# Kernel optimization log

Measured on AMD Instinct MI355X. Metric: run time of the kernel, lower is better.

## Reference

```python
import jax, jax.numpy as jnp
import numpy as np

B, T, C = 1, 1024, 2048
N = 64          # head_size
H = C // N      # 32 heads
D_W = 96        # max(32, round(1.8*sqrt(C)/32)*32)
D_A = 96
D_V = 64        # max(32, round(1.3*sqrt(C)/32)*32)
EPS = 1e-12     # F.normalize eps


def setup_inputs() -> dict:
    key = jax.random.key(0)
    ks = jax.random.split(key, 24)
    g = lambda i, shape, s=0.02: jax.random.normal(ks[i], shape, jnp.float32) * s
    return {
        "x": jax.random.normal(ks[0], (B, T, C), jnp.float32),
        "v_first": jax.random.normal(ks[1], (B, T, C), jnp.float32),
        "attention_mask": jnp.ones((B, T), jnp.float32),
        "w0": g(2, (1, 1, C), 0.1) - 0.5,
        "w1": g(3, (C, D_W)),
        "w2": g(4, (D_W, C)),
        "a0": g(5, (1, 1, C), 0.1),
        "a1": g(6, (C, D_A)),
        "a2": g(7, (D_A, C)),
        "v0": g(8, (1, 1, C), 0.1) + 1.0,
        "v1": g(9, (C, D_V)),
        "v2": g(10, (D_V, C)),
        "k_k": jnp.full((1, 1, C), 0.85, jnp.float32),
        "k_a": jnp.ones((1, 1, C), jnp.float32),
        "r_k": g(11, (H, N), 0.1),
        "Wr": g(12, (C, C)),   # pre-transposed Linear weights: y = x @ W
        "Wk": g(13, (C, C)),
        "Wv": g(14, (C, C)),
        "Wo": g(15, (C, C)),
    }


def rwkv7_scan(r, w, k, v, a, b, mask):
    """RWKV-7 recurrence (RUN_CUDA_RWKV7g). All of r,w,k,v,a,b are (B,T,C); mask (B,T).
    Per head: S_t = S_{t-1}*diag(exp(-exp(w_t))) + (S_{t-1} a_t) b_t^T + v_t k_t^T,
    out_t = S_t r_t.  Masked timesteps leave the state untouched."""
    rh, kh, vh, ah, bh = (t.reshape(B, T, H, N) for t in (r, k, v, a, b))
    dec = jnp.exp(-jnp.exp(w.reshape(B, T, H, N)))
    m = mask[:, :, None, None]
    dec = dec * m + (1.0 - m)            # no decay on padded steps
    kh, vh, ah, bh = kh * m, vh * m, ah * m, bh * m
    seq = tuple(jnp.moveaxis(t, 1, 0) for t in (dec, rh, kh, vh, ah, bh))
    s0 = jnp.zeros((B, H, N, N), r.dtype)  # state[...,i,j]: i=value dim, j=key dim

    def step(state, inp):
        d, rr, kk, vv, aa, bb = inp      # each (B,H,N)
        sa = jnp.einsum('bhij,bhj->bhi', state, aa)
        state = (state * d[:, :, None, :]
                 + sa[..., None] * bb[:, :, None, :]
                 + vv[..., None] * kk[:, :, None, :])
        return state, jnp.einsum('bhij,bhj->bhi', state, rr)

    _, out = jax.lax.scan(step, s0, seq)
    return jnp.moveaxis(out, 0, 1).reshape(B, T, C)


def reference(x, v_first, attention_mask, w0, w1, w2, a0, a1, a2,
              v0, v1, v2, k_k, k_a, r_k, Wr, Wk, Wv, Wo):
    r = x @ Wr
    k = x @ Wk
    v = x @ Wv
    w = -jax.nn.softplus(-(w0 + jnp.tanh(x @ w1) @ w2)) - 0.6
    # layer_id != 0: mix with v_first
    v = v + (v_first - v) * jax.nn.sigmoid(v0 + (x @ v1) @ v2)
    a = jax.nn.sigmoid(a0 + (x @ a1) @ a2)
    kk = k * k_k
    kkh = kk.reshape(B, T, H, N)
    kkh = kkh / jnp.maximum(jnp.linalg.norm(kkh, axis=-1, keepdims=True), EPS)
    kk = kkh.reshape(B, T, C)
    k = k * (1.0 + (a - 1.0) * k_a)
    o = rwkv7_scan(r, w, k, v, -kk, kk * a, attention_mask)
    rh, kh, vh = (t.reshape(B, T, H, N) for t in (r, k, v))
    o = o + ((rh * kh * r_k).sum(-1, keepdims=True) * vh).reshape(B, T, C)
    return (o @ Wo, v_first)
```

## Files before the change

### kernel.cpp

```cpp
#include <hip/hip_runtime.h>
#include <math.h>

#define T_LEN 1024
#define C_DIM 2048
#define H_N   32
#define HEAD  64
#define BTC   (T_LEN * C_DIM)
#define REC2  768
#define RKV_N 6144
#define NPAIR (T_LEN / 2)

typedef __attribute__((ext_vector_type(8))) __bf16 bf16x8;
typedef __attribute__((ext_vector_type(4))) float  f32x4;

__device__ __forceinline__ void gll16(const void* g, void* l) {
    __builtin_amdgcn_global_load_lds((const __attribute__((address_space(1))) void*)g,
                                     (__attribute__((address_space(3))) void*)l, 16, 0, 0);
}

__device__ __forceinline__ float hex_add(float x) {
    int a = __builtin_amdgcn_mov_dpp(__float_as_int(x), 0xB1, 0xF, 0xF, true);
    float y = x + __int_as_float(a);
    int b = __builtin_amdgcn_mov_dpp(__float_as_int(y), 0x4E, 0xF, 0xF, true);
    float z = y + __int_as_float(b);
    int c = __builtin_amdgcn_mov_dpp(__float_as_int(z), 0x141, 0xF, 0xF, true);
    float w = z + __int_as_float(c);
    int d = __builtin_amdgcn_mov_dpp(__float_as_int(w), 0x140, 0xF, 0xF, true);
    return w + __int_as_float(d);
}

__global__ void cast_bf16_k(const float* __restrict__ s, __bf16* __restrict__ d, int n) {
    int i = blockIdx.x * 256 + threadIdx.x;
    if (i < n) d[i] = (__bf16)s[i];
}

__global__ void act_lora1_k(const float* __restrict__ s, __bf16* __restrict__ d) {
    int i = blockIdx.x * 256 + threadIdx.x;
    float v = s[i];
    if ((i & 255) < 96) v = tanhf(v);
    d[i] = (__bf16)v;
}

struct TransBatch {
    const float* s[10];
    __bf16*      d[10];
    int R[10];
    int C[10];
};
__global__ void transpose_batch_k(TransBatch tb) {
    int z = blockIdx.z;
    const float* src = tb.s[z];
    __bf16* dst = tb.d[z];
    int R = tb.R[z], C = tb.C[z];
    int c0 = blockIdx.x * 32, r0 = blockIdx.y * 32;
    if (c0 >= C || r0 >= R) return;
    __shared__ float tile[32][33];
    int tx = threadIdx.x, ty = threadIdx.y;
#pragma unroll
    for (int i = 0; i < 32; i += 8)
        tile[ty + i][tx] = src[(size_t)(r0 + ty + i) * C + c0 + tx];
    __syncthreads();
#pragma unroll
    for (int i = 0; i < 32; i += 8)
        dst[(size_t)(c0 + ty + i) * R + r0 + tx] = (__bf16)tile[tx][ty + i];
}

__global__ __launch_bounds__(256) void gemm_lds_64x128(
    const __bf16* __restrict__ A, const __bf16* __restrict__ BT,
    float* __restrict__ O, int M, int N, int K) {
    __shared__ __bf16 As[64 * 32];
    __shared__ __bf16 Bs[128 * 32];
    int tid  = threadIdx.x;
    int lane = tid & 63;
    int wv   = tid >> 6;
    int m    = lane & 15;
    int q    = lane >> 4;
    int wr   = wv >> 1, wc = wv & 1;
    int row0 = blockIdx.x * 64;
    int col0 = blockIdx.y * 128;

    int srow  = tid >> 2;
    int skoff = (tid & 3) * 8;
    const __bf16* agp = A  + (size_t)(row0 + srow) * K + skoff;
    const __bf16* bgp = BT + (size_t)(col0 + srow) * K + skoff;
    __bf16* alp = As + (size_t)(tid & ~63) * 8;
    __bf16* blp = Bs + (size_t)(tid & ~63) * 8;

    f32x4 acc[2][4];
#pragma unroll
    for (int i = 0; i < 2; i++)
#pragma unroll
        for (int j = 0; j < 4; j++) acc[i][j] = {0.f, 0.f, 0.f, 0.f};

    for (int k0 = 0; k0 < K; k0 += 32) {
        gll16(agp + k0, alp);
        gll16(bgp + k0, blp);
        gll16(bgp + (size_t)64 * K + k0, blp + 64 * 32);
        __syncthreads();

        bf16x8 af[2], bfv[4];
#pragma unroll
        for (int i = 0; i < 2; i++)
            af[i] = *(const bf16x8*)&As[(wr * 32 + i * 16 + m) * 32 + q * 8];
#pragma unroll
        for (int j = 0; j < 4; j++)
            bfv[j] = *(const bf16x8*)&Bs[(wc * 64 + j * 16 + m) * 32 + q * 8];
#pragma unroll
        for (int i = 0; i < 2; i++)
#pragma unroll
            for (int j = 0; j < 4; j++)
                acc[i][j] = __builtin_amdgcn_mfma_f32_16x16x32_bf16(af[i], bfv[j], acc[i][j], 0, 0, 0);
        __syncthreads();
    }

#pragma unroll
    for (int i = 0; i < 2; i++) {
        int orow = row0 + wr * 32 + i * 16 + q * 4;
#pragma unroll
        for (int j = 0; j < 4; j++) {
            int ocol = col0 + wc * 64 + j * 16 + m;
#pragma unroll
            for (int t = 0; t < 4; t++)
                O[(size_t)(orow + t) * N + ocol] = acc[i][j][t];
        }
    }
}

__global__ __launch_bounds__(256) void gemm_lds_128x128(
    const __bf16* __restrict__ A, const __bf16* __restrict__ BT,
    float* __restrict__ O, int M, int N, int K) {
    __shared__ __bf16 As[128 * 32];
    __shared__ __bf16 Bs[128 * 32];
    int tid  = threadIdx.x;
    int lane = tid & 63;
    int wv   = tid >> 6;
    int m    = lane & 15;
    int q    = lane >> 4;
    int row0 = blockIdx.x * 128;
    int col0 = blockIdx.y * 128;

    int srow  = tid >> 2;
    int skoff = (tid & 3) * 8;
    const __bf16* agp = A  + (size_t)(row0 + srow) * K + skoff;
    const __bf16* bgp = BT + (size_t)(col0 + srow) * K + skoff;
    __bf16* alp = As + (size_t)(tid & ~63) * 8;
    __bf16* blp = Bs + (size_t)(tid & ~63) * 8;

    f32x4 acc[2][8];
#pragma unroll
    for (int i = 0; i < 2; i++)
#pragma unroll
        for (int j = 0; j < 8; j++) acc[i][j] = {0.f, 0.f, 0.f, 0.f};

    for (int k0 = 0; k0 < K; k0 += 32) {
        gll16(agp + k0, alp);
        gll16(agp + (size_t)64 * K + k0, alp + 64 * 32);
        gll16(bgp + k0, blp);
        gll16(bgp + (size_t)64 * K + k0, blp + 64 * 32);
        __syncthreads();

        bf16x8 af[2], bfv[8];
#pragma unroll
        for (int i = 0; i < 2; i++)
            af[i] = *(const bf16x8*)&As[(wv * 32 + i * 16 + m) * 32 + q * 8];
#pragma unroll
        for (int j = 0; j < 8; j++)
            bfv[j] = *(const bf16x8*)&Bs[(j * 16 + m) * 32 + q * 8];
#pragma unroll
        for (int i = 0; i < 2; i++)
#pragma unroll
            for (int j = 0; j < 8; j++)
                acc[i][j] = __builtin_amdgcn_mfma_f32_16x16x32_bf16(af[i], bfv[j], acc[i][j], 0, 0, 0);
        __syncthreads();
    }

#pragma unroll
    for (int i = 0; i < 2; i++) {
        int orow = row0 + wv * 32 + i * 16 + q * 4;
#pragma unroll
        for (int j = 0; j < 8; j++) {
            int ocol = col0 + j * 16 + m;
#pragma unroll
            for (int t = 0; t < 4; t++)
                O[(size_t)(orow + t) * N + ocol] = acc[i][j][t];
        }
    }
}

struct Lora2Cfg {
    const __bf16* A[3];
    const __bf16* BT[3];
    float*        O[3];
    int K[3];
};
__global__ __launch_bounds__(256) void gemm_lora2_k(Lora2Cfg cfg) {
    const int LDA = 256, N = C_DIM;
    int z = blockIdx.z;
    const __bf16* A  = cfg.A[z];
    const __bf16* BT = cfg.BT[z];
    float* O = cfg.O[z];
    int K = cfg.K[z];

    __shared__ __bf16 As[64 * 32];
    __shared__ __bf16 Bs[128 * 32];
    int tid  = threadIdx.x;
    int lane = tid & 63;
    int wv   = tid >> 6;
    int m    = lane & 15;
    int q    = lane >> 4;
    int wr   = wv >> 1, wc = wv & 1;
    int row0 = blockIdx.x * 64;
    int col0 = blockIdx.y * 128;

    int srow  = tid >> 2;
    int skoff = (tid & 3) * 8;
    const __bf16* agp = A  + (size_t)(row0 + srow) * LDA + skoff;
    const __bf16* bgp = BT + (size_t)(col0 + srow) * K + skoff;
    __bf16* alp = As + (size_t)(tid & ~63) * 8;
    __bf16* blp = Bs + (size_t)(tid & ~63) * 8;

    f32x4 acc[2][4];
#pragma unroll
    for (int i = 0; i < 2; i++)
#pragma unroll
        for (int j = 0; j < 4; j++) acc[i][j] = {0.f, 0.f, 0.f, 0.f};

    for (int k0 = 0; k0 < K; k0 += 32) {
        gll16(agp + k0, alp);
        gll16(bgp + k0, blp);
        gll16(bgp + (size_t)64 * K + k0, blp + 64 * 32);
        __syncthreads();

        bf16x8 af[2], bfv[4];
#pragma unroll
        for (int i = 0; i < 2; i++)
            af[i] = *(const bf16x8*)&As[(wr * 32 + i * 16 + m) * 32 + q * 8];
#pragma unroll
        for (int j = 0; j < 4; j++)
            bfv[j] = *(const bf16x8*)&Bs[(wc * 64 + j * 16 + m) * 32 + q * 8];
#pragma unroll
        for (int i = 0; i < 2; i++)
#pragma unroll
            for (int j = 0; j < 4; j++)
                acc[i][j] = __builtin_amdgcn_mfma_f32_16x16x32_bf16(af[i], bfv[j], acc[i][j], 0, 0, 0);
        __syncthreads();
    }

#pragma unroll
    for (int i = 0; i < 2; i++) {
        int orow = row0 + wr * 32 + i * 16 + q * 4;
#pragma unroll
        for (int j = 0; j < 4; j++) {
            int ocol = col0 + wc * 64 + j * 16 + m;
#pragma unroll
            for (int t = 0; t < 4; t++)
                O[(size_t)(orow + t) * N + ocol] = acc[i][j][t];
        }
    }
}

__global__ __launch_bounds__(64) void gemm_bt_w16(
    const __bf16* __restrict__ A, const __bf16* __restrict__ BT,
    float* __restrict__ O, int M, int N, int K) {
    int lane = threadIdx.x & 63;
    int m = lane & 15, q = lane >> 4;
    int row0 = blockIdx.x * 16;
    int col0 = blockIdx.y * 16;
    const __bf16* ap = A  + (size_t)(row0 + m) * K + q * 8;
    const __bf16* bp = BT + (size_t)(col0 + m) * K + q * 8;
    f32x4 acc = {0.f,0.f,0.f,0.f};
    for (int k0 = 0; k0 < K; k0 += 32) {
        bf16x8 av = *(const bf16x8*)(ap + k0);
        bf16x8 bv = *(const bf16x8*)(bp + k0);
        acc = __builtin_amdgcn_mfma_f32_16x16x32_bf16(av, bv, acc, 0, 0, 0);
    }
    int orow = row0 + q * 4;
    int ocol = col0 + m;
#pragma unroll
    for (int i = 0; i < 4; i++)
        O[(size_t)(orow + i) * N + ocol] = acc[i];
}

__global__ __launch_bounds__(64) void prep2_k(
    float* __restrict__ rkv,
    const float* __restrict__ vfirst,
    const float* __restrict__ ywb, const float* __restrict__ yab,
    const float* __restrict__ yvb,
    float* __restrict__ pk,
    const float* __restrict__ w0, const float* __restrict__ a0,
    const float* __restrict__ v0, const float* __restrict__ k_k,
    const float* __restrict__ k_a, const float* __restrict__ amask) {
    int tp = blockIdx.x >> 5;
    int h  = blockIdx.x & 31;
    int n  = threadIdx.x;
    int cc = h * HEAD + n;

    float d[2], a[2], bv[2], k[2], v[2], r[2];
#pragma unroll
    for (int s = 0; s < 2; ++s) {
        int t = 2 * tp + s;
        int idx = t * C_DIM + cc;
        size_t idx6 = (size_t)t * RKV_N + cc;
        float m  = amask[t];
        float rr = rkv[idx6];
        float kv = rkv[idx6 + 2048];
        float vv = rkv[idx6 + 4096];
        float wv = w0[cc] + ywb[idx];
        float wfin = -log1pf(expf(-wv)) - 0.6f;
        float dec  = expf(-expf(wfin));
        float sv   = 1.f / (1.f + expf(-(v0[cc] + yvb[idx])));
        float vnew = fmaf(vfirst[idx] - vv, sv, vv);
        float av   = 1.f / (1.f + expf(-(a0[cc] + yab[idx])));
        float kkp  = kv * k_k[cc];
        float ss = kkp * kkp;
#pragma unroll
        for (int off = 32; off > 0; off >>= 1) ss += __shfl_xor(ss, off);
        float kkn  = kkp / fmaxf(sqrtf(ss), 1e-12f);
        float knew = kv * (1.f + (av - 1.f) * k_a[cc]);
        d[s]  = dec * m + (1.f - m);
        a[s]  = -kkn * m;
        bv[s] = kkn * av * m;
        k[s]  = knew * m;
        v[s]  = vnew * m;
        r[s]  = rr;
        rkv[idx6 + 2048] = knew;
        rkv[idx6 + 4096] = vnew;
    }

    float dba = bv[0] * a[1];
    float dka = k[0]  * a[1];
    float dbr = bv[0] * r[0];
    float dkr = k[0]  * r[0];
#pragma unroll
    for (int off = 32; off > 0; off >>= 1) {
        dba += __shfl_xor(dba, off);
        dka += __shfl_xor(dka, off);
        dbr += __shfl_xor(dbr, off);
        dkr += __shfl_xor(dkr, off);
    }

    size_t rec = ((size_t)tp * H_N + h) * REC2;
    pk[rec + n]        = a[0];
    pk[rec + 64 + n]   = d[0] * a[1];
    pk[rec + 128 + n]  = fmaf(dbr, a[0], d[0] * r[0]);
    pk[rec + 192 + n]  = d[0] * d[1];
    pk[rec + 256 + n]  = fmaf(dba, bv[1], d[1] * bv[0]);
    pk[rec + 320 + n]  = bv[1];
    pk[rec + 384 + n]  = fmaf(dka, bv[1], d[1] * k[0]);
    pk[rec + 448 + n]  = k[1];
    pk[rec + 512 + n]  = r[1];
    pk[rec + 576 + n * 3]     = v[0];
    pk[rec + 576 + n * 3 + 1] = v[1];
    pk[rec + 576 + n * 3 + 2] = dkr * v[0];
}

__global__ __launch_bounds__(64, 1) void scan_k(
    const float* __restrict__ pk, float* __restrict__ out) {
    int b = blockIdx.x;
    int xcd  = b & 7;
    int rest = b >> 3;
    int hi   = rest & 3;
    int g    = rest >> 2;
    int h    = xcd + 8 * hi;

    int lane = threadIdx.x;
    int r = lane >> 4;
    int c = lane & 15;
    int row = g * 4 + r;
    int jb  = c * 4;
    int row3 = row * 3;

    float S0 = 0.f, S1 = 0.f, S2 = 0.f, S3 = 0.f;

    float4 A1R[4], A2R[4], R1R[4], DDR[4], B1R[4], B2R[4], C1R[4], C2R[4], R2R[4];
    float3 VRR[4];

    const size_t tstep = (size_t)H_N * REC2;
    const float* base = pk + (size_t)h * REC2;

#define LOADSLOT(S_, T_) do {                          \
    const float* L_ = base + (size_t)(T_) * tstep;     \
    A1R[S_] = *(const float4*)(L_ + jb);               \
    A2R[S_] = *(const float4*)(L_ + 64 + jb);          \
    R1R[S_] = *(const float4*)(L_ + 128 + jb);         \
    DDR[S_] = *(const float4*)(L_ + 192 + jb);         \
    B1R[S_] = *(const float4*)(L_ + 256 + jb);         \
    B2R[S_] = *(const float4*)(L_ + 320 + jb);         \
    C1R[S_] = *(const float4*)(L_ + 384 + jb);         \
    C2R[S_] = *(const float4*)(L_ + 448 + jb);         \
    R2R[S_] = *(const float4*)(L_ + 512 + jb);         \
    VRR[S_] = *(const float3*)(L_ + 576 + row3);       \
} while (0)

#pragma unroll
    for (int s = 0; s < 4; ++s) LOADSLOT(s, s);
    __builtin_amdgcn_sched_barrier(0);

    int off = h * HEAD;

#pragma unroll 1
    for (int tp0 = 0; tp0 < NPAIR; tp0 += 4) {
#pragma unroll
        for (int s = 0; s < 4; ++s) {
            int tp = tp0 + s;
            float4 A1v = A1R[s], A2v = A2R[s], R1v = R1R[s], DDv = DDR[s];
            float4 B1v = B1R[s], B2v = B2R[s], C1v = C1R[s], C2v = C2R[s];
            float4 R2v = R2R[s];
            float3 vr = VRR[s];
            int tn = tp + 4;
            if (tn > NPAIR - 1) tn = NPAIR - 1;
            LOADSLOT(s, tn);
            __builtin_amdgcn_sched_barrier(0);

            float vv1 = vr.x, vv2 = vr.y;
            float pa = fmaf(S0, A1v.x, S1 * A1v.y);
            float qa = fmaf(S2, A1v.z, S3 * A1v.w);
            float pb = fmaf(S0, A2v.x, S1 * A2v.y);
            float qb = fmaf(S2, A2v.z, S3 * A2v.w);
            float pr = fmaf(S0, R1v.x, S1 * R1v.y);
            float qr = fmaf(S2, R1v.z, S3 * R1v.w);
            float sa1 = hex_add(pa + qa);
            float sa2 = hex_add(pb + qb);
            float so1 = hex_add(pr + qr);
            if (c == 0) out[off + row] = so1 + vr.z;

            float t0c = fmaf(vv1, C1v.x, vv2 * C2v.x);
            float t1c = fmaf(vv1, C1v.y, vv2 * C2v.y);
            float t2c = fmaf(vv1, C1v.z, vv2 * C2v.z);
            float t3c = fmaf(vv1, C1v.w, vv2 * C2v.w);
            float z0 = fmaf(sa1, B1v.x, t0c);
            float z1 = fmaf(sa1, B1v.y, t1c);
            float z2 = fmaf(sa1, B1v.z, t2c);
            float z3 = fmaf(sa1, B1v.w, t3c);
            float y0 = fmaf(sa2, B2v.x, z0);
            float y1 = fmaf(sa2, B2v.y, z1);
            float y2 = fmaf(sa2, B2v.z, z2);
            float y3 = fmaf(sa2, B2v.w, z3);
            S0 = fmaf(DDv.x, S0, y0);
            S1 = fmaf(DDv.y, S1, y1);
            S2 = fmaf(DDv.z, S2, y2);
            S3 = fmaf(DDv.w, S3, y3);

            float o0 = fmaf(S0, R2v.x, S1 * R2v.y);
            float o1 = fmaf(S2, R2v.z, S3 * R2v.w);
            float op = hex_add(o0 + o1);
            if (c == 0) out[off + C_DIM + row] = op;
            off += 2 * C_DIM;
            __builtin_amdgcn_sched_barrier(0);
        }
    }
#undef LOADSLOT
}

__global__ __launch_bounds__(64) void resid_k(
    const float* __restrict__ rkv, const float* __restrict__ souts,
    const float* __restrict__ r_k, const float* __restrict__ vfirst,
    __bf16* __restrict__ ob, float* __restrict__ dout) {
    int t = blockIdx.x >> 5;
    int h = blockIdx.x & 31;
    int n = threadIdx.x;
    int cc  = h * HEAD + n;
    int idx = t * C_DIM + cc;
    size_t idx6 = (size_t)t * RKV_N + cc;
    float s = rkv[idx6] * rkv[idx6 + 2048] * r_k[cc];
#pragma unroll
    for (int off = 32; off > 0; off >>= 1) s += __shfl_xor(s, off);
    float ov = souts[idx] + s * rkv[idx6 + 4096];
    ob[idx] = (__bf16)ov;
    dout[BTC + idx] = vfirst[idx];
}

extern "C" void kernel_launch(void* const* d_in, const int* in_sizes, int n_in,
                              void* d_out, int out_size, void* d_ws, size_t ws_size,
                              hipStream_t stream) {
    const float* x      = (const float*)d_in[0];
    const float* vfirst = (const float*)d_in[1];
    const float* amask  = (const float*)d_in[2];
    const float* w0 = (const float*)d_in[3];
    const float* w1 = (const float*)d_in[4];
    const float* w2 = (const float*)d_in[5];
    const float* a0 = (const float*)d_in[6];
    const float* a1 = (const float*)d_in[7];
    const float* a2 = (const float*)d_in[8];
    const float* v0 = (const float*)d_in[9];
    const float* v1 = (const float*)d_in[10];
    const float* v2 = (const float*)d_in[11];
    const float* k_k = (const float*)d_in[12];
    const float* k_a = (const float*)d_in[13];
    const float* r_k = (const float*)d_in[14];
    const float* Wr = (const float*)d_in[15];
    const float* Wk = (const float*)d_in[16];
    const float* Wv = (const float*)d_in[17];
    const float* Wo = (const float*)d_in[18];
    float* dout = (float*)d_out;

    char* wp = (char*)d_ws;
    auto alloc = [&](size_t bytes) -> void* {
        void* p = (void*)wp;
        wp += (bytes + 255) & ~(size_t)255;
        return p;
    };
    __bf16* xb     = (__bf16*)alloc((size_t)BTC * 2);
    __bf16* rkvT   = (__bf16*)alloc((size_t)3 * C_DIM * C_DIM * 2);
    __bf16* WoT    = (__bf16*)alloc((size_t)C_DIM * C_DIM * 2);
    __bf16* lora1T = (__bf16*)alloc((size_t)256 * C_DIM * 2);
    __bf16* w2T = (__bf16*)alloc((size_t)C_DIM * 96 * 2);
    __bf16* a2T = (__bf16*)alloc((size_t)C_DIM * 96 * 2);
    __bf16* v2T = (__bf16*)alloc((size_t)C_DIM * 64 * 2);
    float*  rkv = (float*)alloc((size_t)T_LEN * RKV_N * 4);
    float*  hall  = (float*)alloc((size_t)T_LEN * 256 * 4);
    __bf16* hallb = (__bf16*)alloc((size_t)T_LEN * 256 * 2);
    float*  ywb = (float*)alloc((size_t)BTC * 4);
    float*  yab = (float*)alloc((size_t)BTC * 4);
    float*  yvb = (float*)alloc((size_t)BTC * 4);
    float*  pk  = (float*)alloc((size_t)NPAIR * H_N * REC2 * 4 + 4096);
    float*  souts = (float*)alloc((size_t)BTC * 4);
    __bf16* ob  = (__bf16*)alloc((size_t)BTC * 2);

    cast_bf16_k<<<dim3(BTC / 256), 256, 0, stream>>>(x, xb, BTC);

    TransBatch tb;
    tb.s[0] = Wr; tb.d[0] = rkvT;                              tb.R[0] = C_DIM; tb.C[0] = C_DIM;
    tb.s[1] = Wk; tb.d[1] = rkvT + (size_t)C_DIM * C_DIM;      tb.R[1] = C_DIM; tb.C[1] = C_DIM;
    tb.s[2] = Wv; tb.d[2] = rkvT + (size_t)2 * C_DIM * C_DIM;  tb.R[2] = C_DIM; tb.C[2] = C_DIM;
    tb.s[3] = Wo; tb.d[3] = WoT;                               tb.R[3] = C_DIM; tb.C[3] = C_DIM;
    tb.s[4] = w1; tb.d[4] = lora1T;                            tb.R[4] = C_DIM; tb.C[4] = 96;
    tb.s[5] = a1; tb.d[5] = lora1T + (size_t)96 * C_DIM;       tb.R[5] = C_DIM; tb.C[5] = 96;
    tb.s[6] = v1; tb.d[6] = lora1T + (size_t)192 * C_DIM;      tb.R[6] = C_DIM; tb.C[6] = 64;
    tb.s[7] = w2; tb.d[7] = w2T;                               tb.R[7] = 96;    tb.C[7] = C_DIM;
    tb.s[8] = a2; tb.d[8] = a2T;                               tb.R[8] = 96;    tb.C[8] = C_DIM;
    tb.s[9] = v2; tb.d[9] = v2T;                               tb.R[9] = 64;    tb.C[9] = C_DIM;
    transpose_batch_k<<<dim3(64, 64, 10), dim3(32, 8), 0, stream>>>(tb);

    gemm_lds_128x128<<<dim3(8, 48), 256, 0, stream>>>(xb, rkvT, rkv, T_LEN, RKV_N, C_DIM);

    gemm_bt_w16<<<dim3(64, 16), 64, 0, stream>>>(xb, lora1T, hall, T_LEN, 256, C_DIM);

    act_lora1_k<<<dim3(T_LEN * 256 / 256), 256, 0, stream>>>(hall, hallb);

    Lora2Cfg lc;
    lc.A[0] = hallb;       lc.BT[0] = w2T; lc.O[0] = ywb; lc.K[0] = 96;
    lc.A[1] = hallb + 96;  lc.BT[1] = a2T; lc.O[1] = yab; lc.K[1] = 96;
    lc.A[2] = hallb + 192; lc.BT[2] = v2T; lc.O[2] = yvb; lc.K[2] = 64;
    gemm_lora2_k<<<dim3(16, 16, 3), 256, 0, stream>>>(lc);

    prep2_k<<<dim3(NPAIR * H_N), 64, 0, stream>>>(rkv, vfirst, ywb, yab, yvb,
                                                  pk, w0, a0, v0, k_k, k_a, amask);

    scan_k<<<dim3(H_N * 16), 64, 0, stream>>>(pk, souts);

    resid_k<<<dim3(T_LEN * H_N), 64, 0, stream>>>(rkv, souts, r_k, vfirst, ob, dout);

    gemm_lds_64x128<<<dim3(16, 16), 256, 0, stream>>>(ob, WoT, dout, T_LEN, C_DIM, C_DIM);
}
```

Baseline: 473.2 us.

## Stream scan records through an LDS ring via async global-to-LDS DMA

The scan kernel stops prefetching each timestep record straight into a four-deep register set. It now issues global_load_lds DMA copies into an 8-slot LDS ring, waits on explicit vmcnt values, and reads the next record from LDS into double-buffered registers. Per-step output writes go to an LDS staging buffer and are flushed with coalesced stores at the end. The packed record layout is changed so v pairs and the gate term are contiguous for the new reads. The aim is deeper load latency hiding and fewer scattered global stores, at the cost of LDS traffic and fragile hand-set waitcnt encodings.

```diff
diff --git a/kernel.cpp b/kernel.cpp
--- a/kernel.cpp
+++ b/kernel.cpp
@@ -12,6 +12,9 @@
 
 typedef __attribute__((ext_vector_type(8))) __bf16 bf16x8;
 typedef __attribute__((ext_vector_type(4))) float  f32x4;
+
+#define WAIT_VM18  20338
+#define WAIT_VM21  20341
 
 __device__ __forceinline__ void gll16(const void* g, void* l) {
     __builtin_amdgcn_global_load_lds((const __attribute__((address_space(1))) void*)g,
@@ -349,9 +352,9 @@
     pk[rec + 384 + n]  = fmaf(dka, bv[1], d[1] * k[0]);
     pk[rec + 448 + n]  = k[1];
     pk[rec + 512 + n]  = r[1];
-    pk[rec + 576 + n * 3]     = v[0];
-    pk[rec + 576 + n * 3 + 1] = v[1];
-    pk[rec + 576 + n * 3 + 2] = dkr * v[0];
+    pk[rec + 576 + 2 * n]     = v[0];
+    pk[rec + 576 + 2 * n + 1] = v[1];
+    pk[rec + 704 + n]         = dkr * v[0];
 }
 
 __global__ __launch_bounds__(64, 1) void scan_k(
@@ -368,88 +371,126 @@
     int c = lane & 15;
     int row = g * 4 + r;
     int jb  = c * 4;
-    int row3 = row * 3;
+
+    __shared__ float slab[8][768];
+    __shared__ float lds_out[4096];
 
     float S0 = 0.f, S1 = 0.f, S2 = 0.f, S3 = 0.f;
 
-    float4 A1R[4], A2R[4], R1R[4], DDR[4], B1R[4], B2R[4], C1R[4], C2R[4], R2R[4];
-    float3 VRR[4];
+    struct RegSet {
+        f32x4 A1, A2, R1, DD, B1, B2, C1, C2, R2;
+        float2 v12;
+        float gv;
+    };
+    RegSet RA, RB;
 
     const size_t tstep = (size_t)H_N * REC2;
-    const float* base = pk + (size_t)h * REC2;
-
-#define LOADSLOT(S_, T_) do {                          \
-    const float* L_ = base + (size_t)(T_) * tstep;     \
-    A1R[S_] = *(const float4*)(L_ + jb);               \
-    A2R[S_] = *(const float4*)(L_ + 64 + jb);          \
-    R1R[S_] = *(const float4*)(L_ + 128 + jb);         \
-    DDR[S_] = *(const float4*)(L_ + 192 + jb);         \
-    B1R[S_] = *(const float4*)(L_ + 256 + jb);         \
-    B2R[S_] = *(const float4*)(L_ + 320 + jb);         \
-    C1R[S_] = *(const float4*)(L_ + 384 + jb);         \
-    C2R[S_] = *(const float4*)(L_ + 448 + jb);         \
-    R2R[S_] = *(const float4*)(L_ + 512 + jb);         \
-    VRR[S_] = *(const float3*)(L_ + 576 + row3);       \
+    const float* gbase = pk + (size_t)h * REC2 + lane * 4;
+
+#define DMA3(S_, P_) do {                                     \
+    const float* src_ = gbase + (size_t)(P_) * tstep;         \
+    gll16(src_,       &slab[S_][0]);                          \
+    gll16(src_ + 256, &slab[S_][256]);                        \
+    gll16(src_ + 512, &slab[S_][512]);                        \
 } while (0)
 
-#pragma unroll
-    for (int s = 0; s < 4; ++s) LOADSLOT(s, s);
+#define DSREAD(S_, R_) do {                                   \
+    const float* L_ = &slab[S_][0];                           \
+    R_.A1 = *(const f32x4*)(L_ + jb);                         \
+    R_.A2 = *(const f32x4*)(L_ + 64 + jb);                    \
+    R_.R1 = *(const f32x4*)(L_ + 128 + jb);                   \
+    R_.DD = *(const f32x4*)(L_ + 192 + jb);                   \
+    R_.B1 = *(const f32x4*)(L_ + 256 + jb);                   \
+    R_.B2 = *(const f32x4*)(L_ + 320 + jb);                   \
+    R_.C1 = *(const f32x4*)(L_ + 384 + jb);                   \
+    R_.C2 = *(const f32x4*)(L_ + 448 + jb);                   \
+    R_.R2 = *(const f32x4*)(L_ + 512 + jb);                   \
+    R_.v12 = *(const float2*)(L_ + 576 + 2 * row);            \
+    R_.gv  = L_[704 + row];                                   \
+} while (0)
+
+#define COMPUTE(R_, TP_) do {                                               \
+    float vv1 = R_.v12.x, vv2 = R_.v12.y;                                   \
+    float pa = fmaf(S0, R_.A1[0], S1 * R_.A1[1]);                           \
+    float qa = fmaf(S2, R_.A1[2], S3 * R_.A1[3]);                           \
+    float pb = fmaf(S0, R_.A2[0], S1 * R_.A2[1]);                           \
+    float qb = fmaf(S2, R_.A2[2], S3 * R_.A2[3]);                           \
+    float pr = fmaf(S0, R_.R1[0], S1 * R_.R1[1]);                           \
+    float qr = fmaf(S2, R_.R1[2], S3 * R_.R1[3]);                           \
+    float sa1 = hex_add(pa + qa);                                           \
+    float sa2 = hex_add(pb + qb);                                           \
+    float so1 = hex_add(pr + qr);                                           \
+    float o1v = so1 + R_.gv;                                                \
+    float t0c = fmaf(vv1, R_.C1[0], vv2 * R_.C2[0]);                        \
+    float t1c = fmaf(vv1, R_.C1[1], vv2 * R_.C2[1]);                        \
+    float t2c = fmaf(vv1, R_.C1[2], vv2 * R_.C2[2]);                        \
+    float t3c = fmaf(vv1, R_.C1[3], vv2 * R_.C2[3]);                        \
+    float z0 = fmaf(sa1, R_.B1[0], t0c);                                    \
+    float z1 = fmaf(sa1, R_.B1[1], t1c);                                    \
+    float z2 = fmaf(sa1, R_.B1[2], t2c);                                    \
+    float z3 = fmaf(sa1, R_.B1[3], t3c);                                    \
+    float y0 = fmaf(sa2, R_.B2[0], z0);                                     \
+    float y1 = fmaf(sa2, R_.B2[1], z1);                                     \
+    float y2 = fmaf(sa2, R_.B2[2], z2);                                     \
+    float y3 = fmaf(sa2, R_.B2[3], z3);                                     \
+    S0 = fmaf(R_.DD[0], S0, y0);                                            \
+    S1 = fmaf(R_.DD[1], S1, y1);                                            \
+    S2 = fmaf(R_.DD[2], S2, y2);                                            \
+    S3 = fmaf(R_.DD[3], S3, y3);                                            \
+    float o0 = fmaf(S0, R_.R2[0], S1 * R_.R2[1]);                           \
+    float o1 = fmaf(S2, R_.R2[2], S3 * R_.R2[3]);                           \
+    float op = hex_add(o0 + o1);                                            \
+    if (c == 0) {                                                           \
+        lds_out[(TP_) * 8 + r * 2]     = o1v;                               \
+        lds_out[(TP_) * 8 + r * 2 + 1] = op;                                \
+    }                                                                       \
+} while (0)
+
+#pragma unroll
+    for (int s = 0; s < 8; ++s) DMA3(s, s);
+
+    __builtin_amdgcn_s_waitcnt(WAIT_VM21);
     __builtin_amdgcn_sched_barrier(0);
-
-    int off = h * HEAD;
+    DSREAD(0, RA);
+    __builtin_amdgcn_s_waitcnt(WAIT_VM18);
+    __builtin_amdgcn_sched_barrier(0);
+    DSREAD(1, RB);
+    COMPUTE(RA, 0);
+    DMA3(0, 8);
 
 #pragma unroll 1
-    for (int tp0 = 0; tp0 < NPAIR; tp0 += 4) {
-#pragma unroll
-        for (int s = 0; s < 4; ++s) {
-            int tp = tp0 + s;
-            float4 A1v = A1R[s], A2v = A2R[s], R1v = R1R[s], DDv = DDR[s];
-            float4 B1v = B1R[s], B2v = B2R[s], C1v = C1R[s], C2v = C2R[s];
-            float4 R2v = R2R[s];
-            float3 vr = VRR[s];
-            int tn = tp + 4;
-            if (tn > NPAIR - 1) tn = NPAIR - 1;
-            LOADSLOT(s, tn);
-            __builtin_amdgcn_sched_barrier(0);
-
-            float vv1 = vr.x, vv2 = vr.y;
-            float pa = fmaf(S0, A1v.x, S1 * A1v.y);
-            float qa = fmaf(S2, A1v.z, S3 * A1v.w);
-            float pb = fmaf(S0, A2v.x, S1 * A2v.y);
-            float qb = fmaf(S2, A2v.z, S3 * A2v.w);
-            float pr = fmaf(S0, R1v.x, S1 * R1v.y);
-            float qr = fmaf(S2, R1v.z, S3 * R1v.w);
-            float sa1 = hex_add(pa + qa);
-            float sa2 = hex_add(pb + qb);
-            float so1 = hex_add(pr + qr);
-            if (c == 0) out[off + row] = so1 + vr.z;
-
-            float t0c = fmaf(vv1, C1v.x, vv2 * C2v.x);
-            float t1c = fmaf(vv1, C1v.y, vv2 * C2v.y);
-            float t2c = fmaf(vv1, C1v.z, vv2 * C2v.z);
-            float t3c = fmaf(vv1, C1v.w, vv2 * C2v.w);
-            float z0 = fmaf(sa1, B1v.x, t0c);
-            float z1 = fmaf(sa1, B1v.y, t1c);
-            float z2 = fmaf(sa1, B1v.z, t2c);
-            float z3 = fmaf(sa1, B1v.w, t3c);
-            float y0 = fmaf(sa2, B2v.x, z0);
-            float y1 = fmaf(sa2, B2v.y, z1);
-            float y2 = fmaf(sa2, B2v.z, z2);
-            float y3 = fmaf(sa2, B2v.w, z3);
-            S0 = fmaf(DDv.x, S0, y0);
-            S1 = fmaf(DDv.y, S1, y1);
-            S2 = fmaf(DDv.z, S2, y2);
-            S3 = fmaf(DDv.w, S3, y3);
-
-            float o0 = fmaf(S0, R2v.x, S1 * R2v.y);
-            float o1 = fmaf(S2, R2v.z, S3 * R2v.w);
-            float op = hex_add(o0 + o1);
-            if (c == 0) out[off + C_DIM + row] = op;
-            off += 2 * C_DIM;
-            __builtin_amdgcn_sched_barrier(0);
+    for (int t = 2; t < NPAIR; t += 2) {
+        __builtin_amdgcn_s_waitcnt(WAIT_VM18);
+        __builtin_amdgcn_sched_barrier(0);
+        DSREAD(t & 7, RA);
+        COMPUTE(RB, t - 1);
+        {
+            int p = t + 7; if (p > NPAIR - 1) p = NPAIR - 1;
+            DMA3((t - 1) & 7, p);
         }
-    }
-#undef LOADSLOT
+        __builtin_amdgcn_s_waitcnt(WAIT_VM18);
+        __builtin_amdgcn_sched_barrier(0);
+        DSREAD((t + 1) & 7, RB);
+        COMPUTE(RA, t);
+        {
+            int p = t + 8; if (p > NPAIR - 1) p = NPAIR - 1;
+            DMA3(t & 7, p);
+        }
+    }
+    COMPUTE(RB, NPAIR - 1);
+#undef COMPUTE
+#undef DSREAD
+#undef DMA3
+
+    int colbase = h * HEAD + g * 4;
+#pragma unroll 1
+    for (int i = 0; i < 64; ++i) {
+        int j  = i * 64 + lane;
+        int t  = j >> 2;
+        int r2 = j & 3;
+        out[(size_t)t * C_DIM + colbase + r2] =
+            lds_out[(t >> 1) * 8 + r2 * 2 + (t & 1)];
+    }
 }
 
 __global__ __launch_bounds__(64) void resid_k(
```

New measurement: 512.9 us. +8.4%, slower.

## Fuse four RWKV timesteps per scan iteration via precomputed quad-step coefficients

Applied to the files above, without the earlier changes.

Extends the algebraic chunking of the recurrence from pairs of timesteps to groups of four. The prep kernel now precomputes the combined decay, rank-4 a/b update vectors, readout vectors and value corrections for each quad, so the serial scan advances the state four steps per iteration with fewer dependent cross-lane reductions per timestep. The cost is a larger per-quad record (1600 floats), more shuffle reductions in prep, more register pressure, and a shallower prefetch depth in the scan (2 slots instead of 4).

```diff
diff --git a/kernel.cpp b/kernel.cpp
--- a/kernel.cpp
+++ b/kernel.cpp
@@ -6,9 +6,9 @@
 #define H_N   32
 #define HEAD  64
 #define BTC   (T_LEN * C_DIM)
-#define REC2  768
+#define REC4  1600
 #define RKV_N 6144
-#define NPAIR (T_LEN / 2)
+#define NQ    (T_LEN / 4)
 
 typedef __attribute__((ext_vector_type(8))) __bf16 bf16x8;
 typedef __attribute__((ext_vector_type(4))) float  f32x4;
@@ -281,7 +281,7 @@
         O[(size_t)(orow + i) * N + ocol] = acc[i];
 }
 
-__global__ __launch_bounds__(64) void prep2_k(
+__global__ __launch_bounds__(64) void prep4_k(
     float* __restrict__ rkv,
     const float* __restrict__ vfirst,
     const float* __restrict__ ywb, const float* __restrict__ yab,
@@ -290,15 +290,15 @@
     const float* __restrict__ w0, const float* __restrict__ a0,
     const float* __restrict__ v0, const float* __restrict__ k_k,
     const float* __restrict__ k_a, const float* __restrict__ amask) {
-    int tp = blockIdx.x >> 5;
+    int tq = blockIdx.x >> 5;
     int h  = blockIdx.x & 31;
     int n  = threadIdx.x;
     int cc = h * HEAD + n;
 
-    float d[2], a[2], bv[2], k[2], v[2], r[2];
-#pragma unroll
-    for (int s = 0; s < 2; ++s) {
-        int t = 2 * tp + s;
+    float d[4], a[4], b[4], k[4], v[4], r[4];
+#pragma unroll
+    for (int s = 0; s < 4; ++s) {
+        int t = 4 * tq + s;
         int idx = t * C_DIM + cc;
         size_t idx6 = (size_t)t * RKV_N + cc;
         float m  = amask[t];
@@ -317,41 +317,77 @@
         for (int off = 32; off > 0; off >>= 1) ss += __shfl_xor(ss, off);
         float kkn  = kkp / fmaxf(sqrtf(ss), 1e-12f);
         float knew = kv * (1.f + (av - 1.f) * k_a[cc]);
-        d[s]  = dec * m + (1.f - m);
-        a[s]  = -kkn * m;
-        bv[s] = kkn * av * m;
-        k[s]  = knew * m;
-        v[s]  = vnew * m;
-        r[s]  = rr;
+        d[s] = dec * m + (1.f - m);
+        a[s] = -kkn * m;
+        b[s] = kkn * av * m;
+        k[s] = knew * m;
+        v[s] = vnew * m;
+        r[s] = rr;
         rkv[idx6 + 2048] = knew;
         rkv[idx6 + 4096] = vnew;
     }
 
-    float dba = bv[0] * a[1];
-    float dka = k[0]  * a[1];
-    float dbr = bv[0] * r[0];
-    float dkr = k[0]  * r[0];
-#pragma unroll
-    for (int off = 32; off > 0; off >>= 1) {
-        dba += __shfl_xor(dba, off);
-        dka += __shfl_xor(dka, off);
-        dbr += __shfl_xor(dbr, off);
-        dkr += __shfl_xor(dkr, off);
-    }
-
-    size_t rec = ((size_t)tp * H_N + h) * REC2;
-    pk[rec + n]        = a[0];
-    pk[rec + 64 + n]   = d[0] * a[1];
-    pk[rec + 128 + n]  = fmaf(dbr, a[0], d[0] * r[0]);
-    pk[rec + 192 + n]  = d[0] * d[1];
-    pk[rec + 256 + n]  = fmaf(dba, bv[1], d[1] * bv[0]);
-    pk[rec + 320 + n]  = bv[1];
-    pk[rec + 384 + n]  = fmaf(dka, bv[1], d[1] * k[0]);
-    pk[rec + 448 + n]  = k[1];
-    pk[rec + 512 + n]  = r[1];
-    pk[rec + 576 + n * 3]     = v[0];
-    pk[rec + 576 + n * 3 + 1] = v[1];
-    pk[rec + 576 + n * 3 + 2] = dkr * v[0];
+    float dA[8] = {b[0]*a[1], k[0]*a[1], b[0]*r[0], k[0]*r[0],
+                   b[2]*a[3], k[2]*a[3], b[2]*r[2], k[2]*r[2]};
+#pragma unroll
+    for (int off = 32; off > 0; off >>= 1)
+#pragma unroll
+        for (int i = 0; i < 8; ++i) dA[i] += __shfl_xor(dA[i], off);
+    float da1 = dA[0], dk1 = dA[1], dbr1 = dA[2], dkr1 = dA[3];
+    float da2 = dA[4], dk2 = dA[5], dbr3 = dA[6], dkr3 = dA[7];
+
+    float DDa = d[0] * d[1], DDb = d[2] * d[3];
+    float Ba1 = fmaf(da1, b[1], d[1] * b[0]);
+    float Ba2 = b[1];
+    float Ca1 = fmaf(dk1, b[1], d[1] * k[0]);
+    float Ca2 = k[1];
+    float Ab1 = a[2];
+    float Ab2 = d[2] * a[3];
+    float Bb1 = fmaf(da2, b[3], d[3] * b[2]);
+    float Bb2 = b[3];
+    float Cb1 = fmaf(dk2, b[3], d[3] * k[2]);
+    float Cb2 = k[3];
+    float u3  = fmaf(dbr3, a[2], d[2] * r[2]);
+
+    float dB[16] = {Ba1*Ab1, Ba1*Ab2, Ba2*Ab1, Ba2*Ab2,
+                    Ca1*Ab1, Ca1*Ab2, Ca2*Ab1, Ca2*Ab2,
+                    Ba1*r[1], Ba2*r[1], Ca1*r[1], Ca2*r[1],
+                    Ba1*u3,  Ba2*u3,  Ca1*u3,  Ca2*u3};
+#pragma unroll
+    for (int off = 32; off > 0; off >>= 1)
+#pragma unroll
+        for (int i = 0; i < 16; ++i) dB[i] += __shfl_xor(dB[i], off);
+    float t11 = dB[0], t12 = dB[1], t21 = dB[2], t22 = dB[3];
+    float s11 = dB[4], s12 = dB[5], s21 = dB[6], s22 = dB[7];
+    float p1  = dB[8], p2  = dB[9], q1  = dB[10], q2 = dB[11];
+    float w1  = dB[12], w2 = dB[13], x1 = dB[14], x2 = dB[15];
+
+    float A2v = d[0] * a[1];
+    size_t rec = ((size_t)tq * H_N + h) * REC4;
+    pk[rec + 0 * 64 + n]  = DDa * DDb;
+    pk[rec + 1 * 64 + n]  = a[0];
+    pk[rec + 2 * 64 + n]  = A2v;
+    pk[rec + 3 * 64 + n]  = DDa * Ab1;
+    pk[rec + 4 * 64 + n]  = DDa * Ab2;
+    pk[rec + 5 * 64 + n]  = fmaf(t11, Bb1, fmaf(t12, Bb2, DDb * Ba1));
+    pk[rec + 6 * 64 + n]  = fmaf(t21, Bb1, fmaf(t22, Bb2, DDb * Ba2));
+    pk[rec + 7 * 64 + n]  = Bb1;
+    pk[rec + 8 * 64 + n]  = Bb2;
+    pk[rec + 9 * 64 + n]  = fmaf(dbr1, a[0], d[0] * r[0]);
+    pk[rec + 10 * 64 + n] = fmaf(p1, a[0], fmaf(p2, A2v, DDa * r[1]));
+    pk[rec + 11 * 64 + n] = fmaf(w1, a[0], fmaf(w2, A2v, DDa * u3));
+    pk[rec + 12 * 64 + n] = r[3];
+    pk[rec + 13 * 64 + n] = fmaf(s11, Bb1, fmaf(s12, Bb2, DDb * Ca1));
+    pk[rec + 14 * 64 + n] = fmaf(s21, Bb1, fmaf(s22, Bb2, DDb * Ca2));
+    pk[rec + 15 * 64 + n] = Cb1;
+    pk[rec + 16 * 64 + n] = Cb2;
+    float4 vq = {v[0], v[1], v[2], v[3]};
+    *(float4*)&pk[rec + 1088 + 4 * n] = vq;
+    float4 oc = {dkr1 * v[0],
+                 fmaf(q1, v[0], q2 * v[1]),
+                 fmaf(x1, v[0], fmaf(x2, v[1], dkr3 * v[2])),
+                 0.f};
+    *(float4*)&pk[rec + 1344 + 4 * n] = oc;
 }
 
 __global__ __launch_bounds__(64, 1) void scan_k(
@@ -368,87 +404,99 @@
     int c = lane & 15;
     int row = g * 4 + r;
     int jb  = c * 4;
-    int row3 = row * 3;
 
     float S0 = 0.f, S1 = 0.f, S2 = 0.f, S3 = 0.f;
 
-    float4 A1R[4], A2R[4], R1R[4], DDR[4], B1R[4], B2R[4], C1R[4], C2R[4], R2R[4];
-    float3 VRR[4];
-
-    const size_t tstep = (size_t)H_N * REC2;
-    const float* base = pk + (size_t)h * REC2;
+    float4 DDR[2], A1R[2], A2R[2], A3R[2], A4R[2];
+    float4 B1R[2], B2R[2], B3R[2], B4R[2];
+    float4 R1R[2], R2R[2], R3R[2], R4R[2];
+    float4 C1R[2], C2R[2], C3R[2], C4R[2];
+    float4 VQR[2], OCR[2];
+
+    const size_t tstep = (size_t)H_N * REC4;
+    const float* base = pk + (size_t)h * REC4;
 
 #define LOADSLOT(S_, T_) do {                          \
     const float* L_ = base + (size_t)(T_) * tstep;     \
-    A1R[S_] = *(const float4*)(L_ + jb);               \
-    A2R[S_] = *(const float4*)(L_ + 64 + jb);          \
-    R1R[S_] = *(const float4*)(L_ + 128 + jb);         \
-    DDR[S_] = *(const float4*)(L_ + 192 + jb);         \
-    B1R[S_] = *(const float4*)(L_ + 256 + jb);         \
-    B2R[S_] = *(const float4*)(L_ + 320 + jb);         \
-    C1R[S_] = *(const float4*)(L_ + 384 + jb);         \
-    C2R[S_] = *(const float4*)(L_ + 448 + jb);         \
-    R2R[S_] = *(const float4*)(L_ + 512 + jb);         \
-    VRR[S_] = *(const float3*)(L_ + 576 + row3);       \
+    DDR[S_] = *(const float4*)(L_ + jb);               \
+    A1R[S_] = *(const float4*)(L_ + 64 + jb);          \
+    A2R[S_] = *(const float4*)(L_ + 128 + jb);         \
+    A3R[S_] = *(const float4*)(L_ + 192 + jb);         \
+    A4R[S_] = *(const float4*)(L_ + 256 + jb);         \
+    B1R[S_] = *(const float4*)(L_ + 320 + jb);         \
+    B2R[S_] = *(const float4*)(L_ + 384 + jb);         \
+    B3R[S_] = *(const float4*)(L_ + 448 + jb);         \
+    B4R[S_] = *(const float4*)(L_ + 512 + jb);         \
+    R1R[S_] = *(const float4*)(L_ + 576 + jb);         \
+    R2R[S_] = *(const float4*)(L_ + 640 + jb);         \
+    R3R[S_] = *(const float4*)(L_ + 704 + jb);         \
+    R4R[S_] = *(const float4*)(L_ + 768 + jb);         \
+    C1R[S_] = *(const float4*)(L_ + 832 + jb);         \
+    C2R[S_] = *(const float4*)(L_ + 896 + jb);         \
+    C3R[S_] = *(const float4*)(L_ + 960 + jb);         \
+    C4R[S_] = *(const float4*)(L_ + 1024 + jb);        \
+    VQR[S_] = *(const float4*)(L_ + 1088 + 4 * row);   \
+    OCR[S_] = *(const float4*)(L_ + 1344 + 4 * row);   \
 } while (0)
 
-#pragma unroll
-    for (int s = 0; s < 4; ++s) LOADSLOT(s, s);
+    LOADSLOT(0, 0);
+    LOADSLOT(1, 1);
     __builtin_amdgcn_sched_barrier(0);
 
     int off = h * HEAD;
 
+#define SCAN_STEP(SS, TQ) do {                                                \
+    float4 DDv = DDR[SS];                                                     \
+    float4 A1v = A1R[SS], A2v = A2R[SS], A3v = A3R[SS], A4v = A4R[SS];        \
+    float4 B1v = B1R[SS], B2v = B2R[SS], B3v = B3R[SS], B4v = B4R[SS];        \
+    float4 R1v = R1R[SS], R2v = R2R[SS], R3v = R3R[SS], R4v = R4R[SS];        \
+    float4 C1v = C1R[SS], C2v = C2R[SS], C3v = C3R[SS], C4v = C4R[SS];        \
+    float4 vq = VQR[SS], oc = OCR[SS];                                        \
+    int tn = (TQ) + 2;                                                        \
+    if (tn > NQ - 1) tn = NQ - 1;                                             \
+    LOADSLOT(SS, tn);                                                         \
+    __builtin_amdgcn_sched_barrier(0);                                        \
+                                             \
+    float sa1 = hex_add(fmaf(S0, A1v.x, S1 * A1v.y) + fmaf(S2, A1v.z, S3 * A1v.w)); \
+    float sa2 = hex_add(fmaf(S0, A2v.x, S1 * A2v.y) + fmaf(S2, A2v.z, S3 * A2v.w)); \
+    float sa3 = hex_add(fmaf(S0, A3v.x, S1 * A3v.y) + fmaf(S2, A3v.z, S3 * A3v.w)); \
+    float sa4 = hex_add(fmaf(S0, A4v.x, S1 * A4v.y) + fmaf(S2, A4v.z, S3 * A4v.w)); \
+    float so1 = hex_add(fmaf(S0, R1v.x, S1 * R1v.y) + fmaf(S2, R1v.z, S3 * R1v.w)); \
+    float so2 = hex_add(fmaf(S0, R2v.x, S1 * R2v.y) + fmaf(S2, R2v.z, S3 * R2v.w)); \
+    float so3 = hex_add(fmaf(S0, R3v.x, S1 * R3v.y) + fmaf(S2, R3v.z, S3 * R3v.w)); \
+    if (c == 0) {                                                             \
+        out[off + row]             = so1 + oc.x;                              \
+        out[off + C_DIM + row]     = so2 + oc.y;                              \
+        out[off + 2 * C_DIM + row] = so3 + oc.z;                              \
+    }                                                                         \
+                               \
+    float t0 = fmaf(vq.x, C1v.x, fmaf(vq.y, C2v.x, fmaf(vq.z, C3v.x, vq.w * C4v.x))); \
+    float t1 = fmaf(vq.x, C1v.y, fmaf(vq.y, C2v.y, fmaf(vq.z, C3v.y, vq.w * C4v.y))); \
+    float t2 = fmaf(vq.x, C1v.z, fmaf(vq.y, C2v.z, fmaf(vq.z, C3v.z, vq.w * C4v.z))); \
+    float t3 = fmaf(vq.x, C1v.w, fmaf(vq.y, C2v.w, fmaf(vq.z, C3v.w, vq.w * C4v.w))); \
+    t0 = fmaf(sa1, B1v.x, fmaf(sa2, B2v.x, fmaf(sa3, B3v.x, fmaf(sa4, B4v.x, t0)))); \
+    t1 = fmaf(sa1, B1v.y, fmaf(sa2, B2v.y, fmaf(sa3, B3v.y, fmaf(sa4, B4v.y, t1)))); \
+    t2 = fmaf(sa1, B1v.z, fmaf(sa2, B2v.z, fmaf(sa3, B3v.z, fmaf(sa4, B4v.z, t2)))); \
+    t3 = fmaf(sa1, B1v.w, fmaf(sa2, B2v.w, fmaf(sa3, B3v.w, fmaf(sa4, B4v.w, t3)))); \
+    S0 = fmaf(DDv.x, S0, t0);                                                 \
+    S1 = fmaf(DDv.y, S1, t1);                                                 \
+    S2 = fmaf(DDv.z, S2, t2);                                                 \
+    S3 = fmaf(DDv.w, S3, t3);                                                 \
+                                                   \
+    float o0 = fmaf(S0, R4v.x, S1 * R4v.y);                                   \
+    float o1 = fmaf(S2, R4v.z, S3 * R4v.w);                                   \
+    float op = hex_add(o0 + o1);                                              \
+    if (c == 0) out[off + 3 * C_DIM + row] = op;                              \
+    off += 4 * C_DIM;                                                         \
+    __builtin_amdgcn_sched_barrier(0);                                        \
+} while (0)
+
 #pragma unroll 1
-    for (int tp0 = 0; tp0 < NPAIR; tp0 += 4) {
-#pragma unroll
-        for (int s = 0; s < 4; ++s) {
-            int tp = tp0 + s;
-            float4 A1v = A1R[s], A2v = A2R[s], R1v = R1R[s], DDv = DDR[s];
-            float4 B1v = B1R[s], B2v = B2R[s], C1v = C1R[s], C2v = C2R[s];
-            float4 R2v = R2R[s];
-            float3 vr = VRR[s];
-            int tn = tp + 4;
-            if (tn > NPAIR - 1) tn = NPAIR - 1;
-            LOADSLOT(s, tn);
-            __builtin_amdgcn_sched_barrier(0);
-
-            float vv1 = vr.x, vv2 = vr.y;
-            float pa = fmaf(S0, A1v.x, S1 * A1v.y);
-            float qa = fmaf(S2, A1v.z, S3 * A1v.w);
-            float pb = fmaf(S0, A2v.x, S1 * A2v.y);
-            float qb = fmaf(S2, A2v.z, S3 * A2v.w);
-            float pr = fmaf(S0, R1v.x, S1 * R1v.y);
-            float qr = fmaf(S2, R1v.z, S3 * R1v.w);
-            float sa1 = hex_add(pa + qa);
-            float sa2 = hex_add(pb + qb);
-            float so1 = hex_add(pr + qr);
-            if (c == 0) out[off + row] = so1 + vr.z;
-
-            float t0c = fmaf(vv1, C1v.x, vv2 * C2v.x);
-            float t1c = fmaf(vv1, C1v.y, vv2 * C2v.y);
-            float t2c = fmaf(vv1, C1v.z, vv2 * C2v.z);
-            float t3c = fmaf(vv1, C1v.w, vv2 * C2v.w);
-            float z0 = fmaf(sa1, B1v.x, t0c);
-            float z1 = fmaf(sa1, B1v.y, t1c);
-            float z2 = fmaf(sa1, B1v.z, t2c);
-            float z3 = fmaf(sa1, B1v.w, t3c);
-            float y0 = fmaf(sa2, B2v.x, z0);
-            float y1 = fmaf(sa2, B2v.y, z1);
-            float y2 = fmaf(sa2, B2v.z, z2);
-            float y3 = fmaf(sa2, B2v.w, z3);
-            S0 = fmaf(DDv.x, S0, y0);
-            S1 = fmaf(DDv.y, S1, y1);
-            S2 = fmaf(DDv.z, S2, y2);
-            S3 = fmaf(DDv.w, S3, y3);
-
-            float o0 = fmaf(S0, R2v.x, S1 * R2v.y);
-            float o1 = fmaf(S2, R2v.z, S3 * R2v.w);
-            float op = hex_add(o0 + o1);
-            if (c == 0) out[off + C_DIM + row] = op;
-            off += 2 * C_DIM;
-            __builtin_amdgcn_sched_barrier(0);
-        }
-    }
+    for (int tq0 = 0; tq0 < NQ; tq0 += 2) {
+        SCAN_STEP(0, tq0);
+        SCAN_STEP(1, tq0 + 1);
+    }
+#undef SCAN_STEP
 #undef LOADSLOT
 }
 
@@ -513,7 +561,7 @@
     float*  ywb = (float*)alloc((size_t)BTC * 4);
     float*  yab = (float*)alloc((size_t)BTC * 4);
     float*  yvb = (float*)alloc((size_t)BTC * 4);
-    float*  pk  = (float*)alloc((size_t)NPAIR * H_N * REC2 * 4 + 4096);
+    float*  pk  = (float*)alloc((size_t)NQ * H_N * REC4 * 4 + 4096);
     float*  souts = (float*)alloc((size_t)BTC * 4);
     __bf16* ob  = (__bf16*)alloc((size_t)BTC * 2);
 
@@ -544,8 +592,8 @@
     lc.A[2] = hallb + 192; lc.BT[2] = v2T; lc.O[2] = yvb; lc.K[2] = 64;
     gemm_lora2_k<<<dim3(16, 16, 3), 256, 0, stream>>>(lc);
 
-    prep2_k<<<dim3(NPAIR * H_N), 64, 0, stream>>>(rkv, vfirst, ywb, yab, yvb,
-                                                  pk, w0, a0, v0, k_k, k_a, amask);
+    prep4_k<<<dim3(NQ * H_N), 64, 0, stream>>>(rkv, vfirst, ywb, yab, yvb,
+                                               pk, w0, a0, v0, k_k, k_a, amask);
 
     scan_k<<<dim3(H_N * 16), 64, 0, stream>>>(pk, souts);
 
```

Measured after the change: 471.9 us. No clear change (-0.3%).
